# Kernel tuning notes

Measured on AMD Instinct MI355X. Metric: run time of the kernel, lower is better.

## Reference

```python
import math
import jax, jax.numpy as jnp
import numpy as np

B = 128          # batch_size (graphs)
SEQ = 128        # max_seq_len (nodes per graph)
D = 128          # input_dim
HID = 64         # enc_hidden_dim
HEADS = 4        # in_head
N = B * SEQ      # total nodes
E = 262144       # edges (avg degree 16)


def _make_pe(seq, d):
    pos = np.arange(seq, dtype=np.float32)[:, None]
    i_even = np.arange(0, d, 2, dtype=np.float32)
    pe = np.zeros((seq, d), dtype=np.float32)
    pe[:, 0::2] = np.sin(pos / 10000.0 ** (2.0 * i_even / d))
    pe[:, 1::2] = np.cos(pos / 10000.0 ** (2.0 * (i_even + 1.0) / d))
    return jnp.asarray(pe)


def setup_inputs() -> dict:
    key = jax.random.key(0)
    ks = jax.random.split(key, 10)
    s = 0.1
    return {
        "x": jax.random.normal(ks[0], (N, D), jnp.float32),
        "edge_index": jax.random.randint(ks[1], (2, E), 0, N),
        "pe": _make_pe(SEQ, D),
        "W1": jax.random.normal(ks[2], (D, HEADS * HID), jnp.float32) * s,
        "a_src1": jax.random.normal(ks[3], (HEADS, HID), jnp.float32) * s,
        "a_dst1": jax.random.normal(ks[4], (HEADS, HID), jnp.float32) * s,
        "b1": jnp.zeros((HEADS * HID,), jnp.float32),
        "W2": jax.random.normal(ks[5], (HEADS * HID, HID), jnp.float32) * s,
        "a_src2": jax.random.normal(ks[6], (1, HID), jnp.float32) * s,
        "a_dst2": jax.random.normal(ks[7], (1, HID), jnp.float32) * s,
        "b2": jnp.zeros((HID,), jnp.float32),
        "batch_size": B,
    }


def _gat_conv(x, src, dst, W, a_src, a_dst, b, heads, ch, concat, n):
    # PyG GATConv (eval mode, self-loops already appended to src/dst).
    h = (x @ W).reshape(n, heads, ch)                      # [N,H,C]
    alpha_src = jnp.einsum("nhc,hc->nh", h, a_src)         # [N,H]
    alpha_dst = jnp.einsum("nhc,hc->nh", h, a_dst)
    e = jax.nn.leaky_relu(alpha_src[src] + alpha_dst[dst], 0.2)  # [E,H]
    m = jax.ops.segment_max(e, dst, num_segments=n)        # segment softmax over dst
    ex = jnp.exp(e - m[dst])
    den = jax.ops.segment_sum(ex, dst, num_segments=n)
    alpha = ex / (den[dst] + 1e-16)                        # [E,H]
    out = jax.ops.segment_sum(h[src] * alpha[:, :, None], dst, num_segments=n)
    out = out.reshape(n, heads * ch) if concat else out.mean(axis=1)
    return out + b


def reference(x, edge_index, pe, W1, a_src1, a_dst1, b1, W2, a_src2, a_dst2, b2, batch_size):
    n = x.shape[0]
    loop = jnp.arange(n)
    src = jnp.concatenate([edge_index[0], loop])           # add self-loops (PyG default)
    dst = jnp.concatenate([edge_index[1], loop])
    # positional encoding (dropout inactive in eval)
    h = x * math.sqrt(x.shape[1]) + jnp.tile(pe, (batch_size, 1))
    h = jax.nn.elu(_gat_conv(h, src, dst, W1, a_src1, a_dst1, b1, HEADS, HID, True, n))
    out = _gat_conv(h, src, dst, W2, a_src2, a_dst2, b2, 1, HID, False, n)
    return out.reshape(batch_size, -1, out.shape[1])
```

## Files before the change

### kernel.cpp

```cpp
#include <hip/hip_runtime.h>
#include <hip/hip_bf16.h>

typedef __hip_bfloat16 bf16;

#define N_NODES 16384
#define D_IN    128
#define HID     64
#define HEADS   4
#define F1      256
#define SEQ     128
#define SLOTS   64

__device__ __forceinline__ float wave_sum(float v) {
    #pragma unroll
    for (int o = 32; o > 0; o >>= 1) v += __shfl_xor(v, o, 64);
    return v;
}
__device__ __forceinline__ float wave_max(float v) {
    #pragma unroll
    for (int o = 32; o > 0; o >>= 1) v = fmaxf(v, __shfl_xor(v, o, 64));
    return v;
}
__device__ __forceinline__ float lrelu(float v) { return v > 0.f ? v : 0.2f * v; }
__device__ __forceinline__ float rdlane(float v, int l) {
    return __uint_as_float(__builtin_amdgcn_readlane(__float_as_uint(v), l));
}

__global__ __launch_bounds__(256) void k_gemm1z(const float* __restrict__ x,
                                                const float* __restrict__ pe,
                                                const float* __restrict__ W1,
                                                const float* __restrict__ a_src1,
                                                const float* __restrict__ a_dst1,
                                                bf16* __restrict__ h,
                                                float* __restrict__ as1,
                                                float* __restrict__ ad1,
                                                int4* __restrict__ cntv) {
    int tid = threadIdx.x, lane = tid & 63, wv = tid >> 6;
    if (tid < 4) cntv[blockIdx.x * 4 + tid] = make_int4(0, 0, 0, 0);

    int base = blockIdx.x * 16;
    int j4 = lane * 4;
    float2 xr[4];
    #pragma unroll
    for (int i = 0; i < 4; i++) {
        int row = base + wv * 4 + i;
        float2 xa  = *(const float2*)(x  + (size_t)row * 128 + 2 * lane);
        float2 pea = *(const float2*)(pe + (size_t)(row & (SEQ - 1)) * 128 + 2 * lane);
        xr[i].x = xa.x * 11.313708499f + pea.x;
        xr[i].y = xa.y * 11.313708499f + pea.y;
    }
    float acc[4][4] = {};
    const float4* Wv = (const float4*)W1;
    #pragma unroll 4
    for (int k2 = 0; k2 < 64; k2++) {
        float4 w0 = Wv[(size_t)(2 * k2) * 64 + lane];
        float4 w1 = Wv[(size_t)(2 * k2 + 1) * 64 + lane];
        #pragma unroll
        for (int i = 0; i < 4; i++) {
            float a0 = rdlane(xr[i].x, k2);
            float a1 = rdlane(xr[i].y, k2);
            acc[i][0] += a0 * w0.x + a1 * w1.x;
            acc[i][1] += a0 * w0.y + a1 * w1.y;
            acc[i][2] += a0 * w0.z + a1 * w1.z;
            acc[i][3] += a0 * w0.w + a1 * w1.w;
        }
    }
    float4 asv = *(const float4*)(a_src1 + j4);
    float4 adv = *(const float4*)(a_dst1 + j4);
    #pragma unroll
    for (int i = 0; i < 4; i++) {
        int row = base + wv * 4 + i;
        union { bf16 b[4]; ushort4 u; } cv;
        cv.b[0] = __float2bfloat16(acc[i][0]);
        cv.b[1] = __float2bfloat16(acc[i][1]);
        cv.b[2] = __float2bfloat16(acc[i][2]);
        cv.b[3] = __float2bfloat16(acc[i][3]);
        *(ushort4*)(h + (size_t)row * 256 + j4) = cv.u;
        float vs = acc[i][0] * asv.x + acc[i][1] * asv.y + acc[i][2] * asv.z + acc[i][3] * asv.w;
        float vd = acc[i][0] * adv.x + acc[i][1] * adv.y + acc[i][2] * adv.z + acc[i][3] * adv.w;
        #pragma unroll
        for (int o = 1; o < 16; o <<= 1) {
            vs += __shfl_xor(vs, o);
            vd += __shfl_xor(vd, o);
        }
        if ((lane & 15) == 0) {
            as1[row * 4 + (lane >> 4)] = vs;
            ad1[row * 4 + (lane >> 4)] = vd;
        }
    }
}

__global__ __launch_bounds__(256) void k_scatter(const int* __restrict__ ei, int E, int Etot,
                                                 int* __restrict__ cnt,
                                                 int* __restrict__ esrc) {
    int e = blockIdx.x * 256 + threadIdx.x;
    if (e >= Etot) return;
    int s, d;
    if (e < E) { s = ei[e]; d = ei[E + e]; }
    else       { s = e - E; d = s; }
    int pos = atomicAdd(&cnt[d], 1);
    if (pos < SLOTS) esrc[d * SLOTS + pos] = s;
}

__global__ __launch_bounds__(256) void k_agg1_gemm2(
        const int* __restrict__ cnt, const int* __restrict__ esrc,
        const bf16* __restrict__ h,
        const float* __restrict__ as1, const float* __restrict__ ad1,
        const float* __restrict__ b1,
        const float* __restrict__ W2,
        const float* __restrict__ a_src2, const float* __restrict__ a_dst2,
        bf16* __restrict__ h2, float* __restrict__ as2, float* __restrict__ ad2) {
    __shared__ float hs[8][256];
    int tid = threadIdx.x, lane = tid & 63, wv = tid >> 6;
    int dbase = blockIdx.x * 8;

    int eg = lane >> 3;
    int cg_ = lane & 7;
    const bf16* hbase = h + (size_t)wv * 64 + cg_ * 8;

    for (int it = 0; it < 8; it++) {
        int d = dbase + it;
        int beg = d * SLOTS;
        int deg = min(cnt[d], SLOTS);
        float adw = ad1[d * 4 + wv];

        int s = 0; float ev = -1e30f;
        if (lane < deg) {
            s = esrc[beg + lane];
            ev = lrelu(as1[s * 4 + wv] + adw);
        }
        float mx = wave_max(ev);
        float t = (lane < deg) ? __expf(ev - mx) : 0.f;
        float den = wave_sum(t);

        float acc[8] = {0, 0, 0, 0, 0, 0, 0, 0};
        for (int sub = 0; sub < deg; sub += 32) {
            uint4 u[4]; float te[4];
            #pragma unroll
            for (int q = 0; q < 4; q++) {
                int e = sub + q * 8;
                int se = __shfl(s, e + eg);
                te[q] = __shfl(t, e + eg);
                if (e < deg) u[q] = *(const uint4*)(hbase + (size_t)se * 256);
                else         u[q] = make_uint4(0, 0, 0, 0);
            }
            #pragma unroll
            for (int q = 0; q < 4; q++) {
                acc[0] += te[q] * __uint_as_float(u[q].x << 16);
                acc[1] += te[q] * __uint_as_float(u[q].x & 0xffff0000u);
                acc[2] += te[q] * __uint_as_float(u[q].y << 16);
                acc[3] += te[q] * __uint_as_float(u[q].y & 0xffff0000u);
                acc[4] += te[q] * __uint_as_float(u[q].z << 16);
                acc[5] += te[q] * __uint_as_float(u[q].z & 0xffff0000u);
                acc[6] += te[q] * __uint_as_float(u[q].w << 16);
                acc[7] += te[q] * __uint_as_float(u[q].w & 0xffff0000u);
            }
        }
        #pragma unroll
        for (int j = 0; j < 8; j++) {
            acc[j] += __shfl_xor(acc[j], 8);
            acc[j] += __shfl_xor(acc[j], 16);
            acc[j] += __shfl_xor(acc[j], 32);
        }
        if (lane < 8) {
            float inv = 1.f / (den + 1e-16f);
            int cbase = wv * 64 + lane * 8;
            float o[8];
            #pragma unroll
            for (int j = 0; j < 8; j++) {
                float v = acc[j] * inv + b1[cbase + j];
                o[j] = v > 0.f ? v : (__expf(v) - 1.f);
            }
            float4* dst = (float4*)&hs[it][cbase];
            dst[0] = make_float4(o[0], o[1], o[2], o[3]);
            dst[1] = make_float4(o[4], o[5], o[6], o[7]);
        }
    }
    __syncthreads();

    {
        int r0 = wv * 2, r1 = wv * 2 + 1;
        const float4* h0v = (const float4*)&hs[r0][0];
        const float4* h1v = (const float4*)&hs[r1][0];
        float a0 = 0.f, a1 = 0.f;
        #pragma unroll 4
        for (int k4 = 0; k4 < 64; k4++) {
            float4 u0 = h0v[k4];
            float4 u1 = h1v[k4];
            const float* wp = W2 + (size_t)k4 * 256 + lane;
            float w0 = wp[0], w1 = wp[64], w2 = wp[128], w3 = wp[192];
            a0 += u0.x * w0 + u0.y * w1 + u0.z * w2 + u0.w * w3;
            a1 += u1.x * w0 + u1.y * w1 + u1.z * w2 + u1.w * w3;
        }
        float asj = a_src2[lane], adj = a_dst2[lane];
        int n0 = dbase + r0, n1 = dbase + r1;
        h2[(size_t)n0 * 64 + lane] = __float2bfloat16(a0);
        h2[(size_t)n1 * 64 + lane] = __float2bfloat16(a1);
        float va0 = wave_sum(a0 * asj);
        float vd0 = wave_sum(a0 * adj);
        float va1 = wave_sum(a1 * asj);
        float vd1 = wave_sum(a1 * adj);
        if (lane == 0) {
            as2[n0] = va0; ad2[n0] = vd0;
            as2[n1] = va1; ad2[n1] = vd1;
        }
    }
}

__global__ __launch_bounds__(256) void k_agg2(const int* __restrict__ cnt,
                                              const int* __restrict__ esrc,
                                              const bf16* __restrict__ h2,
                                              const float* __restrict__ as2,
                                              const float* __restrict__ ad2,
                                              const float* __restrict__ b2v,
                                              float* __restrict__ out) {
    int tid = threadIdx.x, lane = tid & 63, wv = tid >> 6;
    int d = blockIdx.x * 4 + wv;
    int beg = d * SLOTS;
    int deg = min(cnt[d], SLOTS);
    float adw = ad2[d];
    int eg = lane >> 3, cg_ = lane & 7;
    const bf16* hbase = h2 + cg_ * 8;

    int s = 0; float ev = -1e30f;
    if (lane < deg) {
        s = esrc[beg + lane];
        ev = lrelu(as2[s] + adw);
    }
    float mx = wave_max(ev);
    float t = (lane < deg) ? __expf(ev - mx) : 0.f;
    float den = wave_sum(t);

    float acc[8] = {0, 0, 0, 0, 0, 0, 0, 0};
    for (int sub = 0; sub < deg; sub += 32) {
        uint4 u[4]; float te[4];
        #pragma unroll
        for (int q = 0; q < 4; q++) {
            int e = sub + q * 8;
            int se = __shfl(s, e + eg);
            te[q] = __shfl(t, e + eg);
            if (e < deg) u[q] = *(const uint4*)(hbase + (size_t)se * 64);
            else         u[q] = make_uint4(0, 0, 0, 0);
        }
        #pragma unroll
        for (int q = 0; q < 4; q++) {
            acc[0] += te[q] * __uint_as_float(u[q].x << 16);
            acc[1] += te[q] * __uint_as_float(u[q].x & 0xffff0000u);
            acc[2] += te[q] * __uint_as_float(u[q].y << 16);
            acc[3] += te[q] * __uint_as_float(u[q].y & 0xffff0000u);
            acc[4] += te[q] * __uint_as_float(u[q].z << 16);
            acc[5] += te[q] * __uint_as_float(u[q].z & 0xffff0000u);
            acc[6] += te[q] * __uint_as_float(u[q].w << 16);
            acc[7] += te[q] * __uint_as_float(u[q].w & 0xffff0000u);
        }
    }
    #pragma unroll
    for (int j = 0; j < 8; j++) {
        acc[j] += __shfl_xor(acc[j], 8);
        acc[j] += __shfl_xor(acc[j], 16);
        acc[j] += __shfl_xor(acc[j], 32);
    }
    if (lane < 8) {
        float inv = 1.f / (den + 1e-16f);
        int cbase = lane * 8;
        float o[8];
        #pragma unroll
        for (int j = 0; j < 8; j++) o[j] = acc[j] * inv + b2v[cbase + j];
        float4* dst = (float4*)(out + (size_t)d * 64 + cbase);
        dst[0] = make_float4(o[0], o[1], o[2], o[3]);
        dst[1] = make_float4(o[4], o[5], o[6], o[7]);
    }
}

extern "C" void kernel_launch(void* const* d_in, const int* in_sizes, int n_in,
                              void* d_out, int out_size, void* d_ws, size_t ws_size,
                              hipStream_t stream) {
    const float* x    = (const float*)d_in[0];
    const int*   ei   = (const int*)  d_in[1];
    const float* pe   = (const float*)d_in[2];
    const float* W1   = (const float*)d_in[3];
    const float* a_s1 = (const float*)d_in[4];
    const float* a_d1 = (const float*)d_in[5];
    const float* b1   = (const float*)d_in[6];
    const float* W2   = (const float*)d_in[7];
    const float* a_s2 = (const float*)d_in[8];
    const float* a_d2 = (const float*)d_in[9];
    const float* b2   = (const float*)d_in[10];

    const int E    = in_sizes[1] / 2;
    const int n    = N_NODES;
    const int Etot = E + n;

    char* p = (char*)d_ws;
    auto alloc = [&](size_t bytes) -> void* {
        void* r = (void*)p;
        p += (bytes + 255) & ~(size_t)255;
        return r;
    };
    int*   cnt     = (int*)  alloc((size_t)n * 4);
    int*   esrc    = (int*)  alloc((size_t)n * SLOTS * 4);
    bf16*  h       = (bf16*) alloc((size_t)n * F1 * 2);
    float* as1     = (float*)alloc((size_t)n * HEADS * 4);
    float* ad1     = (float*)alloc((size_t)n * HEADS * 4);
    bf16*  h2      = (bf16*) alloc((size_t)n * HID * 2);
    float* as2     = (float*)alloc((size_t)n * 4);
    float* ad2     = (float*)alloc((size_t)n * 4);

    int eblocks = (Etot + 255) / 256;

    k_gemm1z    <<<n / 16, 256, 0, stream>>>(x, pe, W1, a_s1, a_d1, h, as1, ad1, (int4*)cnt);
    k_scatter   <<<eblocks, 256, 0, stream>>>(ei, E, Etot, cnt, esrc);
    k_agg1_gemm2<<<n / 8, 256, 0, stream>>>(cnt, esrc, h, as1, ad1, b1,
                                            W2, a_s2, a_d2, h2, as2, ad2);
    k_agg2      <<<n / 4, 256, 0, stream>>>(cnt, esrc, h2, as2, ad2, b2, (float*)d_out);
}
```

Baseline: 180.7 us.

## Co-schedule edge scatter with GEMM1 in one launch and batch softmax prologue

The edge scatter and the first projection GEMM are merged into one grid, with block ranges choosing the role, so the atomic-heavy scatter can run alongside the GEMM instead of after it. Zeroing of the counters moves to a tiny separate kernel, because the fused launch no longer guarantees the counters are cleared before the atomics run. In the layer-1 aggregation, the degree, neighbor-index, logit and softmax work for all 8 destination nodes is hoisted ahead of the feature gathers so the dependent loads can overlap. This raises register pressure and adds one more kernel launch.

```diff
diff --git a/kernel.cpp b/kernel.cpp
--- a/kernel.cpp
+++ b/kernel.cpp
@@ -26,19 +26,29 @@
     return __uint_as_float(__builtin_amdgcn_readlane(__float_as_uint(v), l));
 }
 
-__global__ __launch_bounds__(256) void k_gemm1z(const float* __restrict__ x,
-                                                const float* __restrict__ pe,
-                                                const float* __restrict__ W1,
-                                                const float* __restrict__ a_src1,
-                                                const float* __restrict__ a_dst1,
-                                                bf16* __restrict__ h,
-                                                float* __restrict__ as1,
-                                                float* __restrict__ ad1,
-                                                int4* __restrict__ cntv) {
+__global__ __launch_bounds__(256) void k_zero(int4* p) {
+    p[blockIdx.x * 256 + threadIdx.x] = make_int4(0, 0, 0, 0);
+}
+
+__global__ __launch_bounds__(256) void k_scatter_gemm1(
+        const int* __restrict__ ei, int E, int Etot, int eblocks,
+        int* __restrict__ cnt, int* __restrict__ esrc,
+        const float* __restrict__ x, const float* __restrict__ pe,
+        const float* __restrict__ W1,
+        const float* __restrict__ a_src1, const float* __restrict__ a_dst1,
+        bf16* __restrict__ h, float* __restrict__ as1, float* __restrict__ ad1) {
     int tid = threadIdx.x, lane = tid & 63, wv = tid >> 6;
-    if (tid < 4) cntv[blockIdx.x * 4 + tid] = make_int4(0, 0, 0, 0);
-
-    int base = blockIdx.x * 16;
+    if ((int)blockIdx.x < eblocks) {
+        int e = blockIdx.x * 256 + tid;
+        if (e >= Etot) return;
+        int s, d;
+        if (e < E) { s = ei[e]; d = ei[E + e]; }
+        else       { s = e - E; d = s; }
+        int pos = atomicAdd(&cnt[d], 1);
+        if (pos < SLOTS) esrc[d * SLOTS + pos] = s;
+        return;
+    }
+    int base = (blockIdx.x - eblocks) * 16;
     int j4 = lane * 4;
     float2 xr[4];
     #pragma unroll
@@ -88,18 +98,6 @@
             ad1[row * 4 + (lane >> 4)] = vd;
         }
     }
-}
-
-__global__ __launch_bounds__(256) void k_scatter(const int* __restrict__ ei, int E, int Etot,
-                                                 int* __restrict__ cnt,
-                                                 int* __restrict__ esrc) {
-    int e = blockIdx.x * 256 + threadIdx.x;
-    if (e >= Etot) return;
-    int s, d;
-    if (e < E) { s = ei[e]; d = ei[E + e]; }
-    else       { s = e - E; d = s; }
-    int pos = atomicAdd(&cnt[d], 1);
-    if (pos < SLOTS) esrc[d * SLOTS + pos] = s;
 }
 
 __global__ __launch_bounds__(256) void k_agg1_gemm2(
@@ -118,21 +116,31 @@
     int cg_ = lane & 7;
     const bf16* hbase = h + (size_t)wv * 64 + cg_ * 8;
 
+    int   dgA[8], sA[8];
+    float evA[8], tA[8], dnA[8];
+    #pragma unroll
     for (int it = 0; it < 8; it++) {
-        int d = dbase + it;
-        int beg = d * SLOTS;
-        int deg = min(cnt[d], SLOTS);
-        float adw = ad1[d * 4 + wv];
-
-        int s = 0; float ev = -1e30f;
-        if (lane < deg) {
-            s = esrc[beg + lane];
-            ev = lrelu(as1[s * 4 + wv] + adw);
-        }
-        float mx = wave_max(ev);
-        float t = (lane < deg) ? __expf(ev - mx) : 0.f;
-        float den = wave_sum(t);
-
+        dgA[it] = min(cnt[dbase + it], SLOTS);
+        sA[it]  = (lane < dgA[it]) ? esrc[(dbase + it) * SLOTS + lane] : 0;
+    }
+    #pragma unroll
+    for (int it = 0; it < 8; it++) {
+        float adw = ad1[(dbase + it) * 4 + wv];
+        float av  = (lane < dgA[it]) ? as1[sA[it] * 4 + wv] : 0.f;
+        evA[it] = (lane < dgA[it]) ? lrelu(av + adw) : -1e30f;
+    }
+    #pragma unroll
+    for (int it = 0; it < 8; it++) {
+        float mx = wave_max(evA[it]);
+        float t  = (lane < dgA[it]) ? __expf(evA[it] - mx) : 0.f;
+        dnA[it] = wave_sum(t);
+        tA[it]  = t;
+    }
+
+    #pragma unroll 2
+    for (int it = 0; it < 8; it++) {
+        int deg = dgA[it];
+        int s = sA[it]; float t = tA[it];
         float acc[8] = {0, 0, 0, 0, 0, 0, 0, 0};
         for (int sub = 0; sub < deg; sub += 32) {
             uint4 u[4]; float te[4];
@@ -163,7 +171,7 @@
             acc[j] += __shfl_xor(acc[j], 32);
         }
         if (lane < 8) {
-            float inv = 1.f / (den + 1e-16f);
+            float inv = 1.f / (dnA[it] + 1e-16f);
             int cbase = wv * 64 + lane * 8;
             float o[8];
             #pragma unroll
@@ -308,9 +316,11 @@
 
     int eblocks = (Etot + 255) / 256;
 
-    k_gemm1z    <<<n / 16, 256, 0, stream>>>(x, pe, W1, a_s1, a_d1, h, as1, ad1, (int4*)cnt);
-    k_scatter   <<<eblocks, 256, 0, stream>>>(ei, E, Etot, cnt, esrc);
-    k_agg1_gemm2<<<n / 8, 256, 0, stream>>>(cnt, esrc, h, as1, ad1, b1,
-                                            W2, a_s2, a_d2, h2, as2, ad2);
-    k_agg2      <<<n / 4, 256, 0, stream>>>(cnt, esrc, h2, as2, ad2, b2, (float*)d_out);
-}
+    k_zero         <<<n / (256 * 4), 256, 0, stream>>>((int4*)cnt);
+    k_scatter_gemm1<<<eblocks + n / 16, 256, 0, stream>>>(
+        ei, E, Etot, eblocks, cnt, esrc,
+        x, pe, W1, a_s1, a_d1, h, as1, ad1);
+    k_agg1_gemm2   <<<n / 8, 256, 0, stream>>>(cnt, esrc, h, as1, ad1, b1,
+                                               W2, a_s2, a_d2, h2, as2, ad2);
+    k_agg2         <<<n / 4, 256, 0, stream>>>(cnt, esrc, h2, as2, ad2, b2, (float*)d_out);
+}
```

Result: no change. 181.0 us (+0.2%).
